# Performance work log

Hardware: AMD Instinct MI355X
Metric: run time of the kernel (lower is better)

The kernel has to match this reference:

```python
import jax, jax.numpy as jnp
import numpy as np

N_ATOMS = 50000
DEG = 16
N_EDGES = N_ATOMS * DEG
N_MOL = 1000
NA = 23  # NUMBER_ATOMIC_GRAPH_FEATURES
NB = 7   # NUMBER_BOND_GRAPH_FEATURES


def _sph(v):
    # e3nn-style real spherical harmonics, lmax=2, normalize=False, 'component' normalization
    x, y, z = v[:, 0], v[:, 1], v[:, 2]
    sh1 = jnp.sqrt(3.0) * jnp.stack([x, y, z], axis=-1)  # [E,3] (1o)
    sh2 = jnp.stack([
        jnp.sqrt(15.0) * x * y,
        jnp.sqrt(15.0) * y * z,
        (jnp.sqrt(5.0) / 2.0) * (2 * z * z - x * x - y * y),
        jnp.sqrt(15.0) * x * z,
        (jnp.sqrt(15.0) / 2.0) * (x * x - y * y),
    ], axis=-1)  # [E,5] (2e)
    return sh1, sh2


def setup_inputs() -> dict:
    key = jax.random.key(0)
    ks = jax.random.split(key, 10)
    positions = jax.random.normal(ks[0], (N_ATOMS, 3), jnp.float32)
    x = jax.random.normal(ks[1], (N_ATOMS, NA), jnp.float32)
    edge_attr = jax.random.uniform(ks[2], (N_EDGES, NB), jnp.float32)
    edge_src = jax.random.randint(ks[3], (N_EDGES,), 0, N_ATOMS)
    edge_dst = jnp.repeat(jnp.arange(N_ATOMS), DEG)  # every node has in-degree DEG (required by the module)
    batch = jnp.repeat(jnp.arange(N_MOL), N_ATOMS // N_MOL)
    # tp1: FullyConnectedTensorProduct(NAx0e, 7x0e+7x1o+7x2e -> 32x0e+12x1e+12x1o+8x2e+8x2o)
    # allowed paths: 0e*0e->0e (32), 0e*1o->1o (12), 0e*2e->2e (8); 1e/2o outputs have no path (zero)
    W1_0 = jax.random.normal(ks[4], (NA, NB, 32), jnp.float32)
    W1_1 = jax.random.normal(ks[5], (NA, NB, 12), jnp.float32)
    W1_2 = jax.random.normal(ks[6], (NA, NB, 8), jnp.float32)
    # tp2: paths into 0e: 0e*0e (32x7), 1o*1o (12x7), 2e*2e (8x7)
    W2_0 = jax.random.normal(ks[7], (32, NB, 1), jnp.float32)
    W2_1 = jax.random.normal(ks[8], (12, NB, 1), jnp.float32)
    W2_2 = jax.random.normal(ks[9], (8, NB, 1), jnp.float32)
    return {"positions": positions, "x": x, "edge_attr": edge_attr,
            "W1_0": W1_0, "W1_1": W1_1, "W1_2": W1_2,
            "W2_0": W2_0, "W2_1": W2_1, "W2_2": W2_2,
            "edge_src": edge_src, "edge_dst": edge_dst, "batch": batch}


def reference(positions, x, edge_attr, W1_0, W1_1, W1_2, W2_0, W2_1, W2_2, edge_src, edge_dst, batch):
    N = x.shape[0]
    E = edge_attr.shape[0]
    M = N_MOL
    vec = positions[edge_src] - positions[edge_dst]            # [E,3]
    sh1, sh2 = _sph(vec)
    # FullTensorProduct(7x0e, 0e+1o+2e): scalar block is edge_attr itself; l>0 blocks are outer products
    b1 = edge_attr[:, :, None] * sh1[:, None, :]               # [E,NB,3]
    b2 = edge_attr[:, :, None] * sh2[:, None, :]               # [E,NB,5]
    deg = jax.ops.segment_sum(jnp.ones((E,), positions.dtype), edge_dst, num_segments=N)
    inv_sqrt_deg = 1.0 / jnp.sqrt(deg)                          # all nodes have >=1 edge by construction
    # tp1 on gathered source atom scalars. Since in1 is all-scalar, the SH factor separates:
    t = x[edge_src][:, :, None] * edge_attr[:, None, :]         # [E,NA,NB]
    n1 = 1.0 / np.sqrt(NA * NB)                                 # fan-in normalization
    m0 = jnp.einsum('eab,abo->eo', t, W1_0) * n1                # [E,32] 0e
    m1 = (jnp.einsum('eab,abo->eo', t, W1_1) * n1)[:, :, None] * sh1[:, None, :]  # [E,12,3] 1o
    m2 = (jnp.einsum('eab,abo->eo', t, W1_2) * n1)[:, :, None] * sh2[:, None, :]  # [E,8,5] 2e
    # (tp1's 12x1e and 8x2o outputs are structurally zero and have no path into tp2's 0e output -> dropped)
    s0 = jax.ops.segment_sum(m0, edge_dst, num_segments=N) * inv_sqrt_deg[:, None]
    s1 = jax.ops.segment_sum(m1, edge_dst, num_segments=N) * inv_sqrt_deg[:, None, None]
    s2 = jax.ops.segment_sum(m2, edge_dst, num_segments=N) * inv_sqrt_deg[:, None, None]
    # tp2 -> single 0e; l x l -> 0 contraction is inner product / sqrt(2l+1)
    e0 = jnp.einsum('ea,eb,ab->e', s0[edge_src], edge_attr, W2_0[:, :, 0]) / np.sqrt(32 * NB)
    e1 = jnp.einsum('eam,ebm,ab->e', s1[edge_src], b1, W2_1[:, :, 0]) / (np.sqrt(12 * NB) * np.sqrt(3.0))
    e2 = jnp.einsum('eam,ebm,ab->e', s2[edge_src], b2, W2_2[:, :, 0]) / (np.sqrt(8 * NB) * np.sqrt(5.0))
    edge_out = (e0 + e1 + e2)[:, None]                          # [E,1]
    node_out = jax.ops.segment_sum(edge_out, edge_dst, num_segments=N) * inv_sqrt_deg[:, None]
    apm = jax.ops.segment_sum(jnp.ones((N,), positions.dtype), batch, num_segments=M)
    acc = jax.ops.segment_sum(node_out, batch, num_segments=M)  # [M,1]
    return acc / jnp.sqrt(apm)[:, None]
```

## Files before the change

### kernel.cpp

```cpp
#include <hip/hip_runtime.h>
#include <hip/hip_bf16.h>

#define N_ATOMS 50000
#define DEG 16
#define N_EDGES (N_ATOMS * DEG)
#define N_MOL 1000
#define NA 23
#define NB 7
#define O0 32
#define O1 12
#define O2 8
#define OT 52
#define SROW 128
#define NPW 8
#define WFRAG_N 1792


typedef __attribute__((ext_vector_type(8))) short short8;
typedef __attribute__((ext_vector_type(4))) float floatx4;

__device__ __forceinline__ unsigned short bfbits(float f) {
    unsigned u = __float_as_uint(f);
    u += 0x7FFFu + ((u >> 16) & 1u);
    return (unsigned short)(u >> 16);
}
__device__ __forceinline__ float bf_lo(unsigned u) { return __uint_as_float(u << 16); }
__device__ __forceinline__ float bf_hi(unsigned u) { return __uint_as_float(u & 0xFFFF0000u); }
__device__ __forceinline__ float wred4(float v) {
    v += __shfl_xor(v, 16, 64); v += __shfl_xor(v, 32, 64); return v;
}

__global__ void k_prep(const float* __restrict__ W1_0, const float* __restrict__ W1_1,
                       const float* __restrict__ W1_2, unsigned short* __restrict__ Wfrag,
                       float* __restrict__ out) {
    int idx = blockIdx.x * 256 + threadIdx.x;
    if (idx < N_MOL) out[idx] = 0.0f;
    if (idx >= WFRAG_N * 8) return;
    int j    = idx & 7;
    int lane = (idx >> 3) & 63;
    int st   = idx >> 9;
    int s = st >> 2, t = st & 3;
    int q = lane >> 4, c = lane & 15;
    int b = s, a = q * 8 + j, o = t * 16 + c;
    float val = 0.f;
    if (a < NA && o < OT) {
        const float n1 = 0.07881104062391006f;
        if (o < O0)           val = W1_0[(a * NB + b) * O0 + o] * n1;
        else if (o < O0 + O1) val = W1_1[(a * NB + b) * O1 + (o - O0)] * n1;
        else                  val = W1_2[(a * NB + b) * O2 + (o - O0 - O1)] * n1;
    }
    Wfrag[idx] = bfbits(val);
}

__global__ __launch_bounds__(256, 3) void k2_s(const float* __restrict__ pos,
        const float* __restrict__ x, const float* __restrict__ edge_attr,
        const int* __restrict__ edge_src, const unsigned short* __restrict__ Wfrag,
        unsigned short* __restrict__ sbuf) {
    __shared__ short8 wfrag[WFRAG_N];
    __shared__ float hbuf[4][16][8];
    const int tid  = threadIdx.x;
    const int wid  = tid >> 6;
    const int lane = tid & 63;
    const int lcol = lane & 15;
    const int quad = lane >> 4;

    {
        uint4* dst = (uint4*)wfrag;
        const uint4* src4 = (const uint4*)Wfrag;
        for (int i = tid; i < WFRAG_N; i += 256) dst[i] = src4[i];
    }
    __syncthreads();

    const int wgid = __builtin_amdgcn_readfirstlane(blockIdx.x * 4 + wid);
    const int base = wgid * NPW;
    if (base >= N_ATOMS) return;

    float (*hb)[8] = hbuf[wid];
    const float s3 = 1.7320508075688772f, s15 = 3.872983346207417f;
    const float s5h = 1.118033988749895f, s15h = 1.9364916731037085f;

    auto clampn = [&](int i) { int nn = base + i; return nn < N_ATOMS ? nn : N_ATOMS - 1; };
    int s0v = edge_src[clampn(0) * DEG + lcol];
    int s1v = edge_src[clampn(1) * DEG + lcol];
    float x0[8], e0v[NB];
    #pragma unroll
    for (int j = 0; j < 8; j++) { int a = quad * 8 + j; x0[j] = (a < NA) ? x[s0v * NA + a] : 0.f; }
    {
        const float* p = edge_attr + ((size_t)clampn(0) * DEG + lcol) * NB;
        #pragma unroll
        for (int b = 0; b < NB; b++) e0v[b] = p[b];
    }

    #pragma unroll 1
    for (int i = 0; i < NPW; i++) {
        const int n = base + i;
        if (n >= N_ATOMS) break;
        int s2v = edge_src[clampn(i + 2 < NPW ? i + 2 : i) * DEG + lcol];
        float x1[8], e1v[NB];
        #pragma unroll
        for (int j = 0; j < 8; j++) { int a = quad * 8 + j; x1[j] = (a < NA) ? x[s1v * NA + a] : 0.f; }
        {
            const float* p = edge_attr + ((size_t)clampn(i + 1 < NPW ? i + 1 : i) * DEG + lcol) * NB;
            #pragma unroll
            for (int b = 0; b < NB; b++) e1v[b] = p[b];
        }
        const float pdx = pos[n * 3 + 0], pdy = pos[n * 3 + 1], pdz = pos[n * 3 + 2];
        if (lane < 16) {
            const float vx = pos[s0v * 3 + 0] - pdx;
            const float vy = pos[s0v * 3 + 1] - pdy;
            const float vz = pos[s0v * 3 + 2] - pdz;
            hb[lane][0] = s3 * vx;  hb[lane][1] = s3 * vy;  hb[lane][2] = s3 * vz;
            hb[lane][3] = s15 * vx * vy;
            hb[lane][4] = s15 * vy * vz;
            hb[lane][5] = s5h * (2.f * vz * vz - vx * vx - vy * vy);
            hb[lane][6] = s15 * vx * vz;
            hb[lane][7] = s15h * (vx * vx - vy * vy);
        }
        floatx4 acc0 = {0.f,0.f,0.f,0.f}, acc1 = {0.f,0.f,0.f,0.f};
        floatx4 acc2 = {0.f,0.f,0.f,0.f}, acc3 = {0.f,0.f,0.f,0.f};
        #pragma unroll
        for (int s = 0; s < 7; s++) {
            const float eb = e0v[s];
            union { short8 v; unsigned u[4]; } af;
            #pragma unroll
            for (int j = 0; j < 8; j += 2) {
                float2 pr; pr.x = x0[j] * eb; pr.y = x0[j + 1] * eb;
                __hip_bfloat162 bb = __float22bfloat162_rn(pr);
                af.u[j >> 1] = *(unsigned*)&bb;
            }
            acc0 = __builtin_amdgcn_mfma_f32_16x16x32_bf16(af.v, wfrag[(s*4+0)*64 + lane], acc0, 0, 0, 0);
            acc1 = __builtin_amdgcn_mfma_f32_16x16x32_bf16(af.v, wfrag[(s*4+1)*64 + lane], acc1, 0, 0, 0);
            acc2 = __builtin_amdgcn_mfma_f32_16x16x32_bf16(af.v, wfrag[(s*4+2)*64 + lane], acc2, 0, 0, 0);
            acc3 = __builtin_amdgcn_mfma_f32_16x16x32_bf16(af.v, wfrag[(s*4+3)*64 + lane], acc3, 0, 0, 0);
        }
        float4 hA[4], hB[4];
        #pragma unroll
        for (int r = 0; r < 4; r++) {
            int e = quad * 4 + r;
            hA[r] = *(const float4*)&hb[e][0];
            hB[r] = *(const float4*)&hb[e][4];
        }
        const float q = 0.25f;
        unsigned short* sr = sbuf + (size_t)n * SROW;
        float v0 = wred4(acc0[0] + acc0[1] + acc0[2] + acc0[3]);
        float v1 = wred4(acc1[0] + acc1[1] + acc1[2] + acc1[3]);
        if (quad == 0) { sr[lcol] = bfbits(v0 * q); sr[16 + lcol] = bfbits(v1 * q); }
        if (lcol < 12) {
            float p0 = 0.f, p1 = 0.f, p2 = 0.f;
            #pragma unroll
            for (int r = 0; r < 4; r++) {
                float m = acc2[r];
                p0 += m * hA[r].x; p1 += m * hA[r].y; p2 += m * hA[r].z;
            }
            p0 = wred4(p0); p1 = wred4(p1); p2 = wred4(p2);
            if (quad == 0) {
                sr[32 + lcol] = bfbits(p0 * q);
                sr[44 + lcol] = bfbits(p1 * q);
                sr[56 + lcol] = bfbits(p2 * q);
            }
        } else {
            int a = lcol - 12;
            float p0 = 0.f, p1 = 0.f, p2 = 0.f, p3 = 0.f, p4 = 0.f;
            #pragma unroll
            for (int r = 0; r < 4; r++) {
                float m = acc2[r];
                p0 += m * hA[r].w; p1 += m * hB[r].x; p2 += m * hB[r].y;
                p3 += m * hB[r].z; p4 += m * hB[r].w;
            }
            p0 = wred4(p0); p1 = wred4(p1); p2 = wred4(p2); p3 = wred4(p3); p4 = wred4(p4);
            if (quad == 0) {
                sr[68 + a] = bfbits(p0 * q); sr[76 + a] = bfbits(p1 * q);
                sr[84 + a] = bfbits(p2 * q); sr[92 + a] = bfbits(p3 * q);
                sr[100 + a] = bfbits(p4 * q);
            }
        }
        if (lcol < 4) {
            int a = lcol + 4;
            float p0 = 0.f, p1 = 0.f, p2 = 0.f, p3 = 0.f, p4 = 0.f;
            #pragma unroll
            for (int r = 0; r < 4; r++) {
                float m = acc3[r];
                p0 += m * hA[r].w; p1 += m * hB[r].x; p2 += m * hB[r].y;
                p3 += m * hB[r].z; p4 += m * hB[r].w;
            }
            p0 = wred4(p0); p1 = wred4(p1); p2 = wred4(p2); p3 = wred4(p3); p4 = wred4(p4);
            if (quad == 0) {
                sr[68 + a] = bfbits(p0 * q); sr[76 + a] = bfbits(p1 * q);
                sr[84 + a] = bfbits(p2 * q); sr[92 + a] = bfbits(p3 * q);
                sr[100 + a] = bfbits(p4 * q);
            }
        }
        s0v = s1v; s1v = s2v;
        #pragma unroll
        for (int j = 0; j < 8; j++) x0[j] = x1[j];
        #pragma unroll
        for (int b = 0; b < NB; b++) e0v[b] = e1v[b];
    }
}

__global__ __launch_bounds__(256, 4) void k3_fused(const float* __restrict__ pos,
        const float* __restrict__ edge_attr, const int* __restrict__ edge_src,
        const unsigned short* __restrict__ sbuf,
        const float* __restrict__ W2_0, const float* __restrict__ W2_1,
        const float* __restrict__ W2_2, float* __restrict__ out) {
    __shared__ float ea_t[4][4][16][8];
    __shared__ float hbf[4][4][192];
    const int tid  = threadIdx.x;
    const int wid  = tid >> 6;
    const int lane = tid & 63;
    const int q    = lane >> 4;
    const int e    = lane & 15;
    const int base = __builtin_amdgcn_readfirstlane(blockIdx.x * 4 + wid) * 4;

    const float c0 = 0.06681531047810609f;
    const float c1 = 0.06299407883487121f;
    const float c2 = 0.05976143046671968f;
    int code = 0, aA = 0, aB = 0, valid = 1;
    const float* Wb = W2_0; float norm = c0;
    const int j = lane;
    if (j < 16)      { code = 0; aA = 2 * j;   aB = aA + 1; Wb = W2_0; norm = c0; }
    else if (j < 34) { int g = (j - 16) / 6, r = (j - 16) - 6 * g;
                       code = 1 + g; aA = 2 * r; aB = aA + 1; Wb = W2_1; norm = c1; }
    else if (j < 54) { int g = (j - 34) >> 2, r = (j - 34) & 3;
                       code = 4 + g; aA = 2 * r; aB = aA + 1; Wb = W2_2; norm = c2; }
    else             { valid = 0; }
    float wA[NB], wB[NB];
    #pragma unroll
    for (int b = 0; b < NB; b++) {
        wA[b] = valid ? Wb[aA * NB + b] * norm : 0.f;
        wB[b] = valid ? Wb[aB * NB + b] * norm : 0.f;
    }
    const int jj = valid ? j : 0;

    {
        const int nq = base + q;
        const int sE = edge_src[nq * DEG + e];
        const float* eap = edge_attr + ((size_t)nq * DEG + e) * NB;
        float ev[8];
        #pragma unroll
        for (int b = 0; b < NB; b++) ev[b] = eap[b];
        ev[7] = 0.f;
        const float vx = pos[sE * 3 + 0] - pos[nq * 3 + 0];
        const float vy = pos[sE * 3 + 1] - pos[nq * 3 + 1];
        const float vz = pos[sE * 3 + 2] - pos[nq * 3 + 2];
        float* ed = &ea_t[wid][q][e][0];
        *(float4*)(ed)     = *(float4*)&ev[0];
        *(float4*)(ed + 4) = *(float4*)&ev[4];
        const float s3 = 1.7320508075688772f, s15 = 3.872983346207417f;
        const float s5h = 1.118033988749895f, s15h = 1.9364916731037085f;
        float* hr = &hbf[wid][q][e * 12];
        hr[0] = 1.0f;
        hr[1] = s3 * vx; hr[2] = s3 * vy; hr[3] = s3 * vz;
        hr[4] = s15 * vx * vy;
        hr[5] = s15 * vy * vz;
        hr[6] = s5h * (2.f * vz * vz - vx * vx - vy * vy);
        hr[7] = s15 * vx * vz;
        hr[8] = s15h * (vx * vx - vy * vy);
    }

    const int* srcp = edge_src + (size_t)base * DEG;
    unsigned g0[DEG], g1[DEG];
    #pragma unroll
    for (int k = 0; k < DEG; k++) {
        int s = __builtin_amdgcn_readfirstlane(srcp[k]);
        g0[k] = *(const unsigned*)(sbuf + (size_t)s * SROW + 2 * jj);
    }
    #pragma unroll
    for (int i = 0; i < 4; i++) {
        if (i + 1 < 4) {
            #pragma unroll
            for (int k = 0; k < DEG; k++) {
                int s = __builtin_amdgcn_readfirstlane(srcp[(i + 1) * DEG + k]);
                g1[k] = *(const unsigned*)(sbuf + (size_t)s * SROW + 2 * jj);
            }
        }
        const float* hw = &hbf[wid][i][0];
        float acc = 0.f;
        #pragma unroll
        for (int k = 0; k < DEG; k++) {
            const float4 eA = *(const float4*)&ea_t[wid][i][k][0];
            const float4 eB = *(const float4*)&ea_t[wid][i][k][4];
            const float f = hw[k * 12 + code];
            float we0 = eA.x * wA[0] + eA.y * wA[1] + eA.z * wA[2] + eA.w * wA[3]
                      + eB.x * wA[4] + eB.y * wA[5] + eB.z * wA[6];
            float we1 = eA.x * wB[0] + eA.y * wB[1] + eA.z * wB[2] + eA.w * wB[3]
                      + eB.x * wB[4] + eB.y * wB[5] + eB.z * wB[6];
            acc += f * (bf_lo(g0[k]) * we0 + bf_hi(g0[k]) * we1);
        }
        acc = valid ? acc : 0.f;
        #pragma unroll
        for (int off = 32; off >= 1; off >>= 1) acc += __shfl_xor(acc, off, 64);
        if (lane == 0)
            atomicAdd(out + ((base + i) / 50), acc * 0.035355339059327376f);
        #pragma unroll
        for (int k = 0; k < DEG; k++) g0[k] = g1[k];
    }
}

extern "C" void kernel_launch(void* const* d_in, const int* in_sizes, int n_in,
                              void* d_out, int out_size, void* d_ws, size_t ws_size,
                              hipStream_t stream) {
    const float* pos  = (const float*)d_in[0];
    const float* x    = (const float*)d_in[1];
    const float* ea   = (const float*)d_in[2];
    const float* W1_0 = (const float*)d_in[3];
    const float* W1_1 = (const float*)d_in[4];
    const float* W1_2 = (const float*)d_in[5];
    const float* W2_0 = (const float*)d_in[6];
    const float* W2_1 = (const float*)d_in[7];
    const float* W2_2 = (const float*)d_in[8];
    const int*   esrc = (const int*)d_in[9];
    float* out = (float*)d_out;

    unsigned short* Wfrag = (unsigned short*)d_ws;
    unsigned short* sbuf  = (unsigned short*)((char*)d_ws + 32768);

    hipLaunchKernelGGL(k_prep, dim3(WFRAG_N * 8 / 256), dim3(256), 0, stream,
                       W1_0, W1_1, W1_2, Wfrag, out);
    hipLaunchKernelGGL(k2_s, dim3((N_ATOMS / NPW + 3) / 4), dim3(256), 0, stream,
                       pos, x, ea, esrc, Wfrag, sbuf);
    hipLaunchKernelGGL(k3_fused, dim3(N_ATOMS / 16), dim3(256), 0, stream,
                       pos, ea, esrc, sbuf, W2_0, W2_1, W2_2, out);
}
```

Baseline: 215.1 us.

## Fold weight prep into k2_s, deepen prefetch, preload src indices in k3

Removes the separate k_prep launch: each k2_s block now builds the bf16 MFMA weight fragments in shared memory straight from W1 and also zeroes the output. The k2_s software pipeline is deepened from one to two nodes ahead, and source positions are now prefetched too. k3_fused loads all edge_src indices up front. Launch bounds go up to 4 and 5 blocks. The trade-off is that every block repeats the weight conversion with scattered global reads and pays a larger register footprint, which may cause spills under the tighter bounds. The early-exit check for nodes past N_ATOMS is dropped, which is safe only because N_ATOMS divides evenly.

```diff
diff --git a/kernel.cpp b/kernel.cpp
--- a/kernel.cpp
+++ b/kernel.cpp
@@ -3,7 +3,6 @@
 
 #define N_ATOMS 50000
 #define DEG 16
-#define N_EDGES (N_ATOMS * DEG)
 #define N_MOL 1000
 #define NA 23
 #define NB 7
@@ -30,47 +29,42 @@
     v += __shfl_xor(v, 16, 64); v += __shfl_xor(v, 32, 64); return v;
 }
 
-__global__ void k_prep(const float* __restrict__ W1_0, const float* __restrict__ W1_1,
-                       const float* __restrict__ W1_2, unsigned short* __restrict__ Wfrag,
-                       float* __restrict__ out) {
-    int idx = blockIdx.x * 256 + threadIdx.x;
-    if (idx < N_MOL) out[idx] = 0.0f;
-    if (idx >= WFRAG_N * 8) return;
-    int j    = idx & 7;
-    int lane = (idx >> 3) & 63;
-    int st   = idx >> 9;
-    int s = st >> 2, t = st & 3;
-    int q = lane >> 4, c = lane & 15;
-    int b = s, a = q * 8 + j, o = t * 16 + c;
-    float val = 0.f;
-    if (a < NA && o < OT) {
-        const float n1 = 0.07881104062391006f;
-        if (o < O0)           val = W1_0[(a * NB + b) * O0 + o] * n1;
-        else if (o < O0 + O1) val = W1_1[(a * NB + b) * O1 + (o - O0)] * n1;
-        else                  val = W1_2[(a * NB + b) * O2 + (o - O0 - O1)] * n1;
-    }
-    Wfrag[idx] = bfbits(val);
-}
-
-__global__ __launch_bounds__(256, 3) void k2_s(const float* __restrict__ pos,
+__global__ __launch_bounds__(256, 4) void k2_s(const float* __restrict__ pos,
         const float* __restrict__ x, const float* __restrict__ edge_attr,
-        const int* __restrict__ edge_src, const unsigned short* __restrict__ Wfrag,
-        unsigned short* __restrict__ sbuf) {
+        const int* __restrict__ edge_src,
+        const float* __restrict__ W1_0, const float* __restrict__ W1_1,
+        const float* __restrict__ W1_2,
+        unsigned short* __restrict__ sbuf, float* __restrict__ out) {
     __shared__ short8 wfrag[WFRAG_N];
     __shared__ float hbuf[4][16][8];
     const int tid  = threadIdx.x;
+
+    {
+        int oi = blockIdx.x * 256 + tid;
+        if (oi < N_MOL) out[oi] = 0.0f;
+    }
+    {
+        unsigned short* wf = (unsigned short*)wfrag;
+        const float n1 = 0.07881104062391006f;
+        for (int i = tid; i < WFRAG_N * 8; i += 256) {
+            int j = i & 7, lane8 = (i >> 3) & 63, st = i >> 9;
+            int s = st >> 2, t = st & 3;
+            int a = (lane8 >> 4) * 8 + j, o = t * 16 + (lane8 & 15);
+            float val = 0.f;
+            if (a < NA && o < OT) {
+                if (o < O0)           val = W1_0[(a * NB + s) * O0 + o] * n1;
+                else if (o < O0 + O1) val = W1_1[(a * NB + s) * O1 + (o - O0)] * n1;
+                else                  val = W1_2[(a * NB + s) * O2 + (o - O0 - O1)] * n1;
+            }
+            wf[i] = bfbits(val);
+        }
+    }
+    __syncthreads();
+
     const int wid  = tid >> 6;
     const int lane = tid & 63;
     const int lcol = lane & 15;
     const int quad = lane >> 4;
-
-    {
-        uint4* dst = (uint4*)wfrag;
-        const uint4* src4 = (const uint4*)Wfrag;
-        for (int i = tid; i < WFRAG_N; i += 256) dst[i] = src4[i];
-    }
-    __syncthreads();
-
     const int wgid = __builtin_amdgcn_readfirstlane(blockIdx.x * 4 + wid);
     const int base = wgid * NPW;
     if (base >= N_ATOMS) return;
@@ -79,36 +73,47 @@
     const float s3 = 1.7320508075688772f, s15 = 3.872983346207417f;
     const float s5h = 1.118033988749895f, s15h = 1.9364916731037085f;
 
-    auto clampn = [&](int i) { int nn = base + i; return nn < N_ATOMS ? nn : N_ATOMS - 1; };
-    int s0v = edge_src[clampn(0) * DEG + lcol];
-    int s1v = edge_src[clampn(1) * DEG + lcol];
-    float x0[8], e0v[NB];
-    #pragma unroll
-    for (int j = 0; j < 8; j++) { int a = quad * 8 + j; x0[j] = (a < NA) ? x[s0v * NA + a] : 0.f; }
+    auto nn = [&](int i) { return base + (i < NPW ? i : NPW - 1); };
+    int s0v = edge_src[nn(0) * DEG + lcol];
+    int s1v = edge_src[nn(1) * DEG + lcol];
+    int s2v = edge_src[nn(2) * DEG + lcol];
+    float x0[8], x1[8], ea0[NB], ea1[NB];
+    float p0x, p0y, p0z, p1x, p1y, p1z;
+    #pragma unroll
+    for (int j = 0; j < 8; j++) {
+        int a = quad * 8 + j;
+        x0[j] = (a < NA) ? x[s0v * NA + a] : 0.f;
+        x1[j] = (a < NA) ? x[s1v * NA + a] : 0.f;
+    }
     {
-        const float* p = edge_attr + ((size_t)clampn(0) * DEG + lcol) * NB;
-        #pragma unroll
-        for (int b = 0; b < NB; b++) e0v[b] = p[b];
-    }
+        const float* p = edge_attr + ((size_t)nn(0) * DEG + lcol) * NB;
+        const float* q = edge_attr + ((size_t)nn(1) * DEG + lcol) * NB;
+        #pragma unroll
+        for (int b = 0; b < NB; b++) { ea0[b] = p[b]; ea1[b] = q[b]; }
+    }
+    p0x = pos[s0v * 3 + 0]; p0y = pos[s0v * 3 + 1]; p0z = pos[s0v * 3 + 2];
+    p1x = pos[s1v * 3 + 0]; p1y = pos[s1v * 3 + 1]; p1z = pos[s1v * 3 + 2];
 
     #pragma unroll 1
     for (int i = 0; i < NPW; i++) {
         const int n = base + i;
-        if (n >= N_ATOMS) break;
-        int s2v = edge_src[clampn(i + 2 < NPW ? i + 2 : i) * DEG + lcol];
-        float x1[8], e1v[NB];
-        #pragma unroll
-        for (int j = 0; j < 8; j++) { int a = quad * 8 + j; x1[j] = (a < NA) ? x[s1v * NA + a] : 0.f; }
+        int s3v = edge_src[nn(i + 3) * DEG + lcol];
+        float x2[8], ea2[NB], p2x, p2y, p2z;
+        #pragma unroll
+        for (int j = 0; j < 8; j++) {
+            int a = quad * 8 + j;
+            x2[j] = (a < NA) ? x[s2v * NA + a] : 0.f;
+        }
         {
-            const float* p = edge_attr + ((size_t)clampn(i + 1 < NPW ? i + 1 : i) * DEG + lcol) * NB;
-            #pragma unroll
-            for (int b = 0; b < NB; b++) e1v[b] = p[b];
-        }
+            const float* p = edge_attr + ((size_t)nn(i + 2) * DEG + lcol) * NB;
+            #pragma unroll
+            for (int b = 0; b < NB; b++) ea2[b] = p[b];
+        }
+        p2x = pos[s2v * 3 + 0]; p2y = pos[s2v * 3 + 1]; p2z = pos[s2v * 3 + 2];
+
         const float pdx = pos[n * 3 + 0], pdy = pos[n * 3 + 1], pdz = pos[n * 3 + 2];
         if (lane < 16) {
-            const float vx = pos[s0v * 3 + 0] - pdx;
-            const float vy = pos[s0v * 3 + 1] - pdy;
-            const float vz = pos[s0v * 3 + 2] - pdz;
+            const float vx = p0x - pdx, vy = p0y - pdy, vz = p0z - pdz;
             hb[lane][0] = s3 * vx;  hb[lane][1] = s3 * vy;  hb[lane][2] = s3 * vz;
             hb[lane][3] = s15 * vx * vy;
             hb[lane][4] = s15 * vy * vz;
@@ -120,7 +125,7 @@
         floatx4 acc2 = {0.f,0.f,0.f,0.f}, acc3 = {0.f,0.f,0.f,0.f};
         #pragma unroll
         for (int s = 0; s < 7; s++) {
-            const float eb = e0v[s];
+            const float eb = ea0[s];
             union { short8 v; unsigned u[4]; } af;
             #pragma unroll
             for (int j = 0; j < 8; j += 2) {
@@ -146,59 +151,61 @@
         float v1 = wred4(acc1[0] + acc1[1] + acc1[2] + acc1[3]);
         if (quad == 0) { sr[lcol] = bfbits(v0 * q); sr[16 + lcol] = bfbits(v1 * q); }
         if (lcol < 12) {
-            float p0 = 0.f, p1 = 0.f, p2 = 0.f;
+            float t0 = 0.f, t1 = 0.f, t2 = 0.f;
             #pragma unroll
             for (int r = 0; r < 4; r++) {
                 float m = acc2[r];
-                p0 += m * hA[r].x; p1 += m * hA[r].y; p2 += m * hA[r].z;
-            }
-            p0 = wred4(p0); p1 = wred4(p1); p2 = wred4(p2);
+                t0 += m * hA[r].x; t1 += m * hA[r].y; t2 += m * hA[r].z;
+            }
+            t0 = wred4(t0); t1 = wred4(t1); t2 = wred4(t2);
             if (quad == 0) {
-                sr[32 + lcol] = bfbits(p0 * q);
-                sr[44 + lcol] = bfbits(p1 * q);
-                sr[56 + lcol] = bfbits(p2 * q);
+                sr[32 + lcol] = bfbits(t0 * q);
+                sr[44 + lcol] = bfbits(t1 * q);
+                sr[56 + lcol] = bfbits(t2 * q);
             }
         } else {
             int a = lcol - 12;
-            float p0 = 0.f, p1 = 0.f, p2 = 0.f, p3 = 0.f, p4 = 0.f;
+            float t0 = 0.f, t1 = 0.f, t2 = 0.f, t3 = 0.f, t4 = 0.f;
             #pragma unroll
             for (int r = 0; r < 4; r++) {
                 float m = acc2[r];
-                p0 += m * hA[r].w; p1 += m * hB[r].x; p2 += m * hB[r].y;
-                p3 += m * hB[r].z; p4 += m * hB[r].w;
-            }
-            p0 = wred4(p0); p1 = wred4(p1); p2 = wred4(p2); p3 = wred4(p3); p4 = wred4(p4);
+                t0 += m * hA[r].w; t1 += m * hB[r].x; t2 += m * hB[r].y;
+                t3 += m * hB[r].z; t4 += m * hB[r].w;
+            }
+            t0 = wred4(t0); t1 = wred4(t1); t2 = wred4(t2); t3 = wred4(t3); t4 = wred4(t4);
             if (quad == 0) {
-                sr[68 + a] = bfbits(p0 * q); sr[76 + a] = bfbits(p1 * q);
-                sr[84 + a] = bfbits(p2 * q); sr[92 + a] = bfbits(p3 * q);
-                sr[100 + a] = bfbits(p4 * q);
+                sr[68 + a] = bfbits(t0 * q); sr[76 + a] = bfbits(t1 * q);
+                sr[84 + a] = bfbits(t2 * q); sr[92 + a] = bfbits(t3 * q);
+                sr[100 + a] = bfbits(t4 * q);
             }
         }
         if (lcol < 4) {
             int a = lcol + 4;
-            float p0 = 0.f, p1 = 0.f, p2 = 0.f, p3 = 0.f, p4 = 0.f;
+            float t0 = 0.f, t1 = 0.f, t2 = 0.f, t3 = 0.f, t4 = 0.f;
             #pragma unroll
             for (int r = 0; r < 4; r++) {
                 float m = acc3[r];
-                p0 += m * hA[r].w; p1 += m * hB[r].x; p2 += m * hB[r].y;
-                p3 += m * hB[r].z; p4 += m * hB[r].w;
-            }
-            p0 = wred4(p0); p1 = wred4(p1); p2 = wred4(p2); p3 = wred4(p3); p4 = wred4(p4);
+                t0 += m * hA[r].w; t1 += m * hB[r].x; t2 += m * hB[r].y;
+                t3 += m * hB[r].z; t4 += m * hB[r].w;
+            }
+            t0 = wred4(t0); t1 = wred4(t1); t2 = wred4(t2); t3 = wred4(t3); t4 = wred4(t4);
             if (quad == 0) {
-                sr[68 + a] = bfbits(p0 * q); sr[76 + a] = bfbits(p1 * q);
-                sr[84 + a] = bfbits(p2 * q); sr[92 + a] = bfbits(p3 * q);
-                sr[100 + a] = bfbits(p4 * q);
-            }
-        }
-        s0v = s1v; s1v = s2v;
-        #pragma unroll
-        for (int j = 0; j < 8; j++) x0[j] = x1[j];
-        #pragma unroll
-        for (int b = 0; b < NB; b++) e0v[b] = e1v[b];
-    }
-}
-
-__global__ __launch_bounds__(256, 4) void k3_fused(const float* __restrict__ pos,
+                sr[68 + a] = bfbits(t0 * q); sr[76 + a] = bfbits(t1 * q);
+                sr[84 + a] = bfbits(t2 * q); sr[92 + a] = bfbits(t3 * q);
+                sr[100 + a] = bfbits(t4 * q);
+            }
+        }
+        s0v = s1v; s1v = s2v; s2v = s3v;
+        #pragma unroll
+        for (int j = 0; j < 8; j++) { x0[j] = x1[j]; x1[j] = x2[j]; }
+        #pragma unroll
+        for (int b = 0; b < NB; b++) { ea0[b] = ea1[b]; ea1[b] = ea2[b]; }
+        p0x = p1x; p0y = p1y; p0z = p1z;
+        p1x = p2x; p1y = p2y; p1z = p2z;
+    }
+}
+
+__global__ __launch_bounds__(256, 5) void k3_fused(const float* __restrict__ pos,
         const float* __restrict__ edge_attr, const int* __restrict__ edge_src,
         const unsigned short* __restrict__ sbuf,
         const float* __restrict__ W2_0, const float* __restrict__ W2_1,
@@ -231,6 +238,14 @@
         wB[b] = valid ? Wb[aB * NB + b] * norm : 0.f;
     }
     const int jj = valid ? j : 0;
+
+    const int* srcp = edge_src + (size_t)base * DEG;
+    int ssrc[4][DEG];
+    #pragma unroll
+    for (int i = 0; i < 4; i++)
+        #pragma unroll
+        for (int k = 0; k < DEG; k++)
+            ssrc[i][k] = __builtin_amdgcn_readfirstlane(srcp[i * DEG + k]);
 
     {
         const int nq = base + q;
@@ -258,21 +273,16 @@
         hr[8] = s15h * (vx * vx - vy * vy);
     }
 
-    const int* srcp = edge_src + (size_t)base * DEG;
     unsigned g0[DEG], g1[DEG];
     #pragma unroll
-    for (int k = 0; k < DEG; k++) {
-        int s = __builtin_amdgcn_readfirstlane(srcp[k]);
-        g0[k] = *(const unsigned*)(sbuf + (size_t)s * SROW + 2 * jj);
-    }
+    for (int k = 0; k < DEG; k++)
+        g0[k] = *(const unsigned*)(sbuf + (size_t)ssrc[0][k] * SROW + 2 * jj);
     #pragma unroll
     for (int i = 0; i < 4; i++) {
         if (i + 1 < 4) {
             #pragma unroll
-            for (int k = 0; k < DEG; k++) {
-                int s = __builtin_amdgcn_readfirstlane(srcp[(i + 1) * DEG + k]);
-                g1[k] = *(const unsigned*)(sbuf + (size_t)s * SROW + 2 * jj);
-            }
+            for (int k = 0; k < DEG; k++)
+                g1[k] = *(const unsigned*)(sbuf + (size_t)ssrc[i + 1][k] * SROW + 2 * jj);
         }
         const float* hw = &hbf[wid][i][0];
         float acc = 0.f;
@@ -312,13 +322,10 @@
     const int*   esrc = (const int*)d_in[9];
     float* out = (float*)d_out;
 
-    unsigned short* Wfrag = (unsigned short*)d_ws;
-    unsigned short* sbuf  = (unsigned short*)((char*)d_ws + 32768);
-
-    hipLaunchKernelGGL(k_prep, dim3(WFRAG_N * 8 / 256), dim3(256), 0, stream,
-                       W1_0, W1_1, W1_2, Wfrag, out);
+    unsigned short* sbuf = (unsigned short*)d_ws;
+
     hipLaunchKernelGGL(k2_s, dim3((N_ATOMS / NPW + 3) / 4), dim3(256), 0, stream,
-                       pos, x, ea, esrc, Wfrag, sbuf);
+                       pos, x, ea, esrc, W1_0, W1_1, W1_2, sbuf, out);
     hipLaunchKernelGGL(k3_fused, dim3(N_ATOMS / 16), dim3(256), 0, stream,
                        pos, ea, esrc, sbuf, W2_0, W2_1, W2_2, out);
 }
```

After: 407.1 us. 89.3% more time.
